# Kernel optimization log

Hardware: AMD Instinct MI355X
Metric: run time of the kernel (lower is better)

The kernel has to match this reference:

```python
import jax, jax.numpy as jnp
import numpy as np

D_MODEL = 1024
N_HEADS = 16
D_KV = 64
ROPE_THETA = 10000.0


def setup_inputs() -> dict:
    key = jax.random.key(0)
    k1, k2, k3, k4, k5 = jax.random.split(key, 5)
    B, S = 4, 2048
    scale = 0.02
    return {
        "positions": jnp.arange(S, dtype=jnp.int64 if jax.config.jax_enable_x64 else jnp.int32),
        "hidden_states": jax.random.normal(k1, (B, S, D_MODEL), dtype=jnp.float32),
        "wq": jax.random.normal(k2, (D_MODEL, N_HEADS * D_KV), dtype=jnp.float32) * scale,
        "wk": jax.random.normal(k3, (D_MODEL, N_HEADS * D_KV), dtype=jnp.float32) * scale,
        "wv": jax.random.normal(k4, (D_MODEL, N_HEADS * D_KV), dtype=jnp.float32) * scale,
        "wo": jax.random.normal(k5, (N_HEADS * D_KV, D_MODEL), dtype=jnp.float32) * scale,
    }


def _rope(positions, q, k):
    # Neox-style simple RoPE, matching SimpleRoPE fallback.
    # q, k: [B, H, S, Dh]
    Dh = q.shape[-1]
    inv_freq = 1.0 / (ROPE_THETA ** (jnp.arange(0, Dh, 2, dtype=jnp.float32) / Dh))  # [Dh/2]
    freqs = positions.astype(jnp.float32)[:, None] * inv_freq[None, :]  # [S, Dh/2]
    emb = jnp.concatenate([freqs, freqs], axis=-1)  # [S, Dh]
    cos = jnp.cos(emb)[None, None, :, :]
    sin = jnp.sin(emb)[None, None, :, :]

    def rotate_half(x):
        x1, x2 = jnp.split(x, 2, axis=-1)
        return jnp.concatenate([-x2, x1], axis=-1)

    q_rot = q * cos + rotate_half(q) * sin
    k_rot = k * cos + rotate_half(k) * sin
    return q_rot, k_rot


def reference(positions, hidden_states, wq, wk, wv, wo):
    B, S, _ = hidden_states.shape
    H, Dh = N_HEADS, D_KV

    def split_heads(x):  # [B, S, H*Dh] -> [B, H, S, Dh]
        return x.reshape(B, S, H, Dh).transpose(0, 2, 1, 3)

    q = split_heads(hidden_states @ wq)
    k = split_heads(hidden_states @ wk)
    v = split_heads(hidden_states @ wv)

    q, k = _rope(positions, q, k)

    # scale = 1.0 (no 1/sqrt(d) scaling), matching the source module
    scores = jnp.einsum("bhqd,bhkd->bhqk", q, k)
    attn = jax.nn.softmax(scores.astype(jnp.float32), axis=-1).astype(scores.dtype)
    # dropout is identity in eval mode
    out = jnp.einsum("bhqk,bhkd->bhqd", attn, v)  # [B, H, S, Dh]
    out = out.transpose(0, 2, 1, 3).reshape(B, S, H * Dh)
    return out @ wo
```

## Files before the change

### kernel.cpp

```cpp
#include <hip/hip_runtime.h>
#include <hip/hip_bf16.h>


typedef __bf16 bf16_t;
typedef __bf16 bf16x4 __attribute__((ext_vector_type(4)));
typedef __bf16 bf16x8 __attribute__((ext_vector_type(8)));
typedef float f32x4 __attribute__((ext_vector_type(4)));

#define MFMA16(a, b, c) __builtin_amdgcn_mfma_f32_16x16x32_bf16((a), (b), (c), 0, 0, 0)

#define GLOAD_LDS(gp, lp) \
  __builtin_amdgcn_global_load_lds( \
      (const __attribute__((address_space(1))) void*)(gp), \
      (__attribute__((address_space(3))) void*)(lp), 16, 0, 0)

__global__ __launch_bounds__(256) void cvt_kernel(const float* __restrict__ X,
                                                  bf16_t* __restrict__ Y) {
  const int i = (blockIdx.x * 256 + threadIdx.x) * 4;
  const f32x4 x = *(const f32x4*)(X + i);
  bf16x4 y;
#pragma unroll
  for (int k = 0; k < 4; k++) y[k] = (bf16_t)x[k];
  *(bf16x4*)(Y + i) = y;
}

__global__ __launch_bounds__(256) void wtrans4_kernel(
    const float* __restrict__ w0, const float* __restrict__ w1,
    const float* __restrict__ w2, const float* __restrict__ w3,
    bf16_t* __restrict__ out) {
  __shared__ bf16_t t[32][33];
  const int tx = threadIdx.x, ty = threadIdx.y;
  const int bx = blockIdx.x, by = blockIdx.y, z = blockIdx.z;
  const float* W = (z == 0) ? w0 : (z == 1) ? w1 : (z == 2) ? w2 : w3;
  bf16_t* Wt = out + (size_t)z * 1024 * 1024;
#pragma unroll
  for (int i = ty; i < 32; i += 8)
    t[i][tx] = (bf16_t)W[(size_t)(by * 32 + i) * 1024 + bx * 32 + tx];
  __syncthreads();
#pragma unroll
  for (int i = ty; i < 32; i += 8)
    Wt[(size_t)(bx * 32 + i) * 1024 + by * 32 + tx] = t[tx][i];
}

__global__ __launch_bounds__(256) void vtrans_kernel(const bf16_t* __restrict__ V,
                                                     bf16_t* __restrict__ VT) {
  __shared__ bf16_t t[32][33];
  const int tx = threadIdx.x, ty = threadIdx.y;
  const int sx = blockIdx.x * 32, cy = blockIdx.y * 32, b = blockIdx.z;
  const bf16_t* Vb = V + (size_t)b * 2048 * 1024;
  bf16_t* VTb = VT + (size_t)b * 1024 * 2048;
#pragma unroll
  for (int i = ty; i < 32; i += 8)
    t[i][tx] = Vb[(size_t)(sx + i) * 1024 + cy + tx];
  __syncthreads();
#pragma unroll
  for (int i = ty; i < 32; i += 8)
    VTb[(size_t)(cy + i) * 2048 + sx + tx] = t[tx][i];
}

template <typename TC, bool FUSED_QKV>
__global__ __launch_bounds__(256) void gemm_kernel(
    const bf16_t* __restrict__ A, const bf16_t* __restrict__ BtBase,
    TC* __restrict__ CBase, const int ropeIn) {
  constexpr int K = 1024, N = 1024;
  __shared__ __align__(16) bf16_t As[128 * 32];
  __shared__ __align__(16) bf16_t Bs[128 * 32];

  const int tid = threadIdx.x;
  const int lane = tid & 63, w = tid >> 6;
  const int l15 = lane & 15, quad = lane >> 4;
  const int wm = w >> 1, wn = w & 1;
  const int m0 = blockIdx.x * 128;

  int n0, rope;
  const bf16_t* Bt;
  TC* C;
  if (FUSED_QKV) {
    const int which = blockIdx.y >> 3;
    n0 = (blockIdx.y & 7) * 128;
    Bt = BtBase + (size_t)which * (1u << 20);
    C = CBase + (size_t)which * (8u << 20);
    rope = (which < 2);
  } else {
    n0 = blockIdx.y * 128;
    Bt = BtBase;
    C = CBase;
    rope = ropeIn;
  }

  f32x4 acc[4][4] = {};
  const int li8 = lane >> 3, j = lane & 7;

  for (int k0 = 0; k0 < K; k0 += 32) {
#pragma unroll
    for (int p = 0; p < 2; ++p) {
      const int g = w * 16 + p * 8 + li8;
      const int jp = j ^ (g & 7);
      const int row = 2 * g + (jp >> 2), kb = jp & 3;
      GLOAD_LDS(A + (size_t)(m0 + row) * K + k0 + kb * 8, As + (w * 16 + p * 8) * 64);
      GLOAD_LDS(Bt + (size_t)(n0 + row) * K + k0 + kb * 8, Bs + (w * 16 + p * 8) * 64);
    }
    __syncthreads();

    bf16x8 af[4], bfv[4];
#pragma unroll
    for (int mi = 0; mi < 4; mi++) {
      const int R = wm * 64 + mi * 16 + l15, g = R >> 1;
      const int jj = (((R & 1) << 2) | quad) ^ (g & 7);
      af[mi] = *(const bf16x8*)(As + g * 64 + jj * 8);
    }
#pragma unroll
    for (int ni = 0; ni < 4; ni++) {
      const int R = wn * 64 + ni * 16 + l15, g = R >> 1;
      const int jj = (((R & 1) << 2) | quad) ^ (g & 7);
      bfv[ni] = *(const bf16x8*)(Bs + g * 64 + jj * 8);
    }
#pragma unroll
    for (int mi = 0; mi < 4; mi++)
#pragma unroll
      for (int ni = 0; ni < 4; ni++)
        acc[mi][ni] = MFMA16(af[mi], bfv[ni], acc[mi][ni]);
    __syncthreads();
  }

#pragma unroll
  for (int mi = 0; mi < 4; mi++) {
    const int rbase = m0 + wm * 64 + mi * 16 + quad * 4;
    if (rope) {
#pragma unroll
      for (int r = 0; r < 4; r++) {
        const float pos = (float)((rbase + r) & 2047);
#pragma unroll
        for (int ni = 0; ni < 2; ni++) {
          const int d2 = ni * 16 + l15;
          const float invf = __powf(10000.0f, -(float)d2 * (1.0f / 32.0f));
          float sv, cv;
          __sincosf(pos * invf, &sv, &cv);
          const float a0 = acc[mi][ni][r], a2 = acc[mi][ni + 2][r];
          acc[mi][ni][r] = a0 * cv - a2 * sv;
          acc[mi][ni + 2][r] = a2 * cv + a0 * sv;
        }
      }
    }
#pragma unroll
    for (int ni = 0; ni < 4; ni++) {
      const int c0 = n0 + wn * 64 + ni * 16 + l15;
#pragma unroll
      for (int r = 0; r < 4; r++)
        C[(size_t)(rbase + r) * N + c0] = (TC)acc[mi][ni][r];
    }
  }
}

#define PSTR 72

__global__ __launch_bounds__(256) void attn_kernel(const bf16_t* __restrict__ Q,
                                                   const bf16_t* __restrict__ K,
                                                   const bf16_t* __restrict__ VT,
                                                   bf16_t* __restrict__ O) {
  __shared__ __align__(16) bf16_t Kl[64 * 64];
  __shared__ __align__(16) bf16_t Vl[64 * 64];
  __shared__ __align__(16) bf16_t Pl[4 * 16 * PSTR];

  const int tid = threadIdx.x;
  const int lane = tid & 63, w = tid >> 6;
  const int l15 = lane & 15, quad = lane >> 4;
  const int q0 = blockIdx.x * 64;
  const int bh = blockIdx.y, b = bh >> 4, h = bh & 15;

  const size_t base = (size_t)b * 2048 * 1024 + (size_t)h * 64;
  const bf16_t* Qb = Q + base;
  const bf16_t* Kb = K + base;
  const bf16_t* VTb = VT + (size_t)(b * 1024 + h * 64) * 2048;

  const int qrow = q0 + w * 16 + l15;
  bf16x8 qf[2];
  qf[0] = *(const bf16x8*)(Qb + (size_t)qrow * 1024 + quad * 8);
  qf[1] = *(const bf16x8*)(Qb + (size_t)qrow * 1024 + 32 + quad * 8);

  f32x4 accO[4] = {};
  float lsum[4] = {0.f, 0.f, 0.f, 0.f};

  const int li8 = lane >> 3, j = lane & 7;

  for (int kv0 = 0; kv0 < 2048; kv0 += 64) {
#pragma unroll
    for (int p = 0; p < 2; ++p) {
      const int kr = w * 16 + p * 8 + li8;
      const int blk = j ^ (kr & 7);
      GLOAD_LDS(Kb + (size_t)(kv0 + kr) * 1024 + blk * 8, Kl + (w * 16 + p * 8) * 64);
      GLOAD_LDS(VTb + (size_t)kr * 2048 + kv0 + blk * 8, Vl + (w * 16 + p * 8) * 64);
    }
    __syncthreads();

    f32x4 sc[4] = {};
#pragma unroll
    for (int t = 0; t < 2; t++)
#pragma unroll
      for (int nb = 0; nb < 4; nb++) {
        const int R = nb * 16 + l15;
        const int jj = (t * 4 + quad) ^ (R & 7);
        const bf16x8 kf = *(const bf16x8*)(Kl + R * 64 + jj * 8);
        sc[nb] = MFMA16(qf[t], kf, sc[nb]);
      }

#pragma unroll
    for (int nb = 0; nb < 4; nb++)
#pragma unroll
      for (int r = 0; r < 4; r++) {
        const float p = __expf(sc[nb][r]);
        lsum[r] += p;
        Pl[w * 16 * PSTR + (quad * 4 + r) * PSTR + nb * 16 + l15] = (bf16_t)p;
      }
    __asm__ volatile("s_waitcnt lgkmcnt(0)" ::: "memory");

#pragma unroll
    for (int t = 0; t < 2; t++) {
      const bf16x8 pf = *(const bf16x8*)(Pl + w * 16 * PSTR + l15 * PSTR + t * 32 + quad * 8);
#pragma unroll
      for (int nb = 0; nb < 4; nb++) {
        const int R = nb * 16 + l15;
        const int jj = (t * 4 + quad) ^ (R & 7);
        const bf16x8 vf = *(const bf16x8*)(Vl + R * 64 + jj * 8);
        accO[nb] = MFMA16(pf, vf, accO[nb]);
      }
    }
    __syncthreads();
  }

#pragma unroll
  for (int r = 0; r < 4; r++) {
    float s = lsum[r];
    s += __shfl_xor(s, 1);
    s += __shfl_xor(s, 2);
    s += __shfl_xor(s, 4);
    s += __shfl_xor(s, 8);
    lsum[r] = 1.0f / s;
  }
  bf16_t* Ob = O + base;
#pragma unroll
  for (int r = 0; r < 4; r++) {
    const int qr = q0 + w * 16 + quad * 4 + r;
#pragma unroll
    for (int nb = 0; nb < 4; nb++)
      Ob[(size_t)qr * 1024 + nb * 16 + l15] = (bf16_t)(accO[nb][r] * lsum[r]);
  }
}

extern "C" void kernel_launch(void* const* d_in, const int* in_sizes, int n_in,
                              void* d_out, int out_size, void* d_ws, size_t ws_size,
                              hipStream_t stream) {
  const float* hs = (const float*)d_in[1];
  const float* wq = (const float*)d_in[2];
  const float* wk = (const float*)d_in[3];
  const float* wv = (const float*)d_in[4];
  const float* wo = (const float*)d_in[5];

  char* ws = (char*)d_ws;
  const size_t MB = 1024 * 1024;
  bf16_t* WtQKV = (bf16_t*)(ws + 0 * MB);
  bf16_t* WtO = (bf16_t*)(ws + 6 * MB);
  bf16_t* hsb = (bf16_t*)(ws + 8 * MB);
  bf16_t* VT = (bf16_t*)(ws + 8 * MB);
  bf16_t* Qw = (bf16_t*)(ws + 24 * MB);
  bf16_t* Kw = (bf16_t*)(ws + 40 * MB);
  bf16_t* Vw = (bf16_t*)(ws + 56 * MB);
  bf16_t* Ow = (bf16_t*)(ws + 56 * MB);

  wtrans4_kernel<<<dim3(32, 32, 4), dim3(32, 8), 0, stream>>>(wq, wk, wv, wo, WtQKV);
  cvt_kernel<<<8192, 256, 0, stream>>>(hs, hsb);

  gemm_kernel<bf16_t, true><<<dim3(64, 24), 256, 0, stream>>>(hsb, WtQKV, Qw, 0);

  vtrans_kernel<<<dim3(64, 32, 4), dim3(32, 8), 0, stream>>>(Vw, VT);

  attn_kernel<<<dim3(32, 64), 256, 0, stream>>>(Qw, Kw, VT, Ow);

  gemm_kernel<float, false><<<dim3(64, 8), 256, 0, stream>>>(Ow, WtO, (float*)d_out, 0);
}
```

Measured before the change: 339.9 us.

## Split attention KV across waves with 128-wide tiles and LDS cross-wave reduction

The attention kernel now processes 128 KV rows per iteration, and each of the four waves handles a 32-row KV slice for all 64 queries of the block instead of owning 16 queries. K fragments are reused across four query sub-blocks. Partial outputs and row sums are combined through a shared LDS arena with a rotating accumulation followed by normalisation. This halves the number of loop iterations and barriers and improves MFMA-to-load reuse, but it adds register pressure (a 4x4 accumulator array, with launch_bounds set to 2 blocks), a cross-wave reduction epilogue, and a larger LDS footprint.

New measurement: 931.0 us. +173.9%, slower.

```diff
diff --git a/kernel.cpp b/kernel.cpp
--- a/kernel.cpp
+++ b/kernel.cpp
@@ -152,19 +152,23 @@
   }
 }
 
-#define PSTR 72
-
-__global__ __launch_bounds__(256) void attn_kernel(const bf16_t* __restrict__ Q,
-                                                   const bf16_t* __restrict__ K,
-                                                   const bf16_t* __restrict__ VT,
-                                                   bf16_t* __restrict__ O) {
-  __shared__ __align__(16) bf16_t Kl[64 * 64];
-  __shared__ __align__(16) bf16_t Vl[64 * 64];
-  __shared__ __align__(16) bf16_t Pl[4 * 16 * PSTR];
+#define PLSTR 40
+
+__global__ __launch_bounds__(256, 2) void attn_kernel(const bf16_t* __restrict__ Q,
+                                                      const bf16_t* __restrict__ K,
+                                                      const bf16_t* __restrict__ VT,
+                                                      bf16_t* __restrict__ O) {
+  __shared__ __align__(16) char arena[53248];
+  bf16_t* Kl = (bf16_t*)arena;
+  bf16_t* Vl = (bf16_t*)(arena + 16384);
+  bf16_t* Pl = (bf16_t*)(arena + 32768);
+  float* Obuf = (float*)arena;
+  float* lsumB = (float*)(arena + 32768);
 
   const int tid = threadIdx.x;
   const int lane = tid & 63, w = tid >> 6;
   const int l15 = lane & 15, quad = lane >> 4;
+  const int li8 = lane >> 3, j = lane & 7;
   const int q0 = blockIdx.x * 64;
   const int bh = blockIdx.y, b = bh >> 4, h = bh & 15;
 
@@ -173,77 +177,119 @@
   const bf16_t* Kb = K + base;
   const bf16_t* VTb = VT + (size_t)(b * 1024 + h * 64) * 2048;
 
-  const int qrow = q0 + w * 16 + l15;
-  bf16x8 qf[2];
-  qf[0] = *(const bf16x8*)(Qb + (size_t)qrow * 1024 + quad * 8);
-  qf[1] = *(const bf16x8*)(Qb + (size_t)qrow * 1024 + 32 + quad * 8);
-
-  f32x4 accO[4] = {};
-  float lsum[4] = {0.f, 0.f, 0.f, 0.f};
-
-  const int li8 = lane >> 3, j = lane & 7;
-
-  for (int kv0 = 0; kv0 < 2048; kv0 += 64) {
-#pragma unroll
-    for (int p = 0; p < 2; ++p) {
-      const int kr = w * 16 + p * 8 + li8;
-      const int blk = j ^ (kr & 7);
-      GLOAD_LDS(Kb + (size_t)(kv0 + kr) * 1024 + blk * 8, Kl + (w * 16 + p * 8) * 64);
-      GLOAD_LDS(VTb + (size_t)kr * 2048 + kv0 + blk * 8, Vl + (w * 16 + p * 8) * 64);
-    }
-    __syncthreads();
-
-    f32x4 sc[4] = {};
+  bf16x8 qf[4][2];
+#pragma unroll
+  for (int mb = 0; mb < 4; mb++)
 #pragma unroll
     for (int t = 0; t < 2; t++)
-#pragma unroll
-      for (int nb = 0; nb < 4; nb++) {
-        const int R = nb * 16 + l15;
+      qf[mb][t] = *(const bf16x8*)(Qb + (size_t)(q0 + mb * 16 + l15) * 1024 + t * 32 + quad * 8);
+
+  f32x4 accO[4][4] = {};
+  float lsum[4][4] = {};
+  bf16_t* Plw = Pl + w * (64 * PLSTR);
+
+  for (int kv0 = 0; kv0 < 2048; kv0 += 128) {
+#pragma unroll
+    for (int p = 0; p < 4; ++p) {
+      const int g = w * 32 + p * 8 + li8;
+      const int blk = j ^ (g & 7);
+      GLOAD_LDS(Kb + (size_t)(kv0 + g) * 1024 + blk * 8, Kl + (w * 32 + p * 8) * 64);
+      GLOAD_LDS(VTb + (size_t)(g >> 1) * 2048 + kv0 + (g & 1) * 64 + blk * 8,
+                Vl + (w * 32 + p * 8) * 64);
+    }
+    __syncthreads();
+
+#pragma unroll
+    for (int nb2 = 0; nb2 < 2; nb2++) {
+      f32x4 sc[4] = {};
+#pragma unroll
+      for (int t = 0; t < 2; t++) {
+        const int R = w * 32 + nb2 * 16 + l15;
         const int jj = (t * 4 + quad) ^ (R & 7);
         const bf16x8 kf = *(const bf16x8*)(Kl + R * 64 + jj * 8);
-        sc[nb] = MFMA16(qf[t], kf, sc[nb]);
+#pragma unroll
+        for (int mb = 0; mb < 4; mb++)
+          sc[mb] = MFMA16(qf[mb][t], kf, sc[mb]);
       }
-
-#pragma unroll
-    for (int nb = 0; nb < 4; nb++)
-#pragma unroll
-      for (int r = 0; r < 4; r++) {
-        const float p = __expf(sc[nb][r]);
-        lsum[r] += p;
-        Pl[w * 16 * PSTR + (quad * 4 + r) * PSTR + nb * 16 + l15] = (bf16_t)p;
-      }
+#pragma unroll
+      for (int mb = 0; mb < 4; mb++)
+#pragma unroll
+        for (int r = 0; r < 4; r++) {
+          const float p = __expf(sc[mb][r]);
+          lsum[mb][r] += p;
+          Plw[(mb * 16 + quad * 4 + r) * PLSTR + nb2 * 16 + l15] = (bf16_t)p;
+        }
+    }
     __asm__ volatile("s_waitcnt lgkmcnt(0)" ::: "memory");
 
-#pragma unroll
-    for (int t = 0; t < 2; t++) {
-      const bf16x8 pf = *(const bf16x8*)(Pl + w * 16 * PSTR + l15 * PSTR + t * 32 + quad * 8);
-#pragma unroll
-      for (int nb = 0; nb < 4; nb++) {
-        const int R = nb * 16 + l15;
-        const int jj = (t * 4 + quad) ^ (R & 7);
-        const bf16x8 vf = *(const bf16x8*)(Vl + R * 64 + jj * 8);
-        accO[nb] = MFMA16(pf, vf, accO[nb]);
-      }
-    }
-    __syncthreads();
-  }
-
-#pragma unroll
-  for (int r = 0; r < 4; r++) {
-    float s = lsum[r];
-    s += __shfl_xor(s, 1);
-    s += __shfl_xor(s, 2);
-    s += __shfl_xor(s, 4);
-    s += __shfl_xor(s, 8);
-    lsum[r] = 1.0f / s;
-  }
+    bf16x8 pf[4], vf[4];
+#pragma unroll
+    for (int mb = 0; mb < 4; mb++)
+      pf[mb] = *(const bf16x8*)(Plw + (mb * 16 + l15) * PLSTR + quad * 8);
+#pragma unroll
+    for (int nb = 0; nb < 4; nb++) {
+      const int R = nb * 16 + l15;
+      const int g = R * 2 + (w >> 1);
+      const int jj = ((w & 1) * 4 + quad) ^ (g & 7);
+      vf[nb] = *(const bf16x8*)(Vl + g * 64 + jj * 8);
+    }
+#pragma unroll
+    for (int mb = 0; mb < 4; mb++)
+#pragma unroll
+      for (int nb = 0; nb < 4; nb++)
+        accO[mb][nb] = MFMA16(pf[mb], vf[nb], accO[mb][nb]);
+    __syncthreads();
+  }
+
+#pragma unroll
+  for (int mb = 0; mb < 4; mb++)
+#pragma unroll
+    for (int r = 0; r < 4; r++) {
+      float s = lsum[mb][r];
+      s += __shfl_xor(s, 1);
+      s += __shfl_xor(s, 2);
+      s += __shfl_xor(s, 4);
+      s += __shfl_xor(s, 8);
+      lsum[mb][r] = s;
+    }
+  if (l15 == 0) {
+#pragma unroll
+    for (int mb = 0; mb < 4; mb++)
+#pragma unroll
+      for (int r = 0; r < 4; r++)
+        lsumB[w * 64 + mb * 16 + quad * 4 + r] = lsum[mb][r];
+  }
+
+#pragma unroll
+  for (int p = 0; p < 4; p++) {
+    const int s = (w + p) & 3;
+    if (p == 0) {
+#pragma unroll
+      for (int nb = 0; nb < 4; nb++)
+#pragma unroll
+        for (int r = 0; r < 4; r++)
+          Obuf[(s * 16 + quad * 4 + r) * 68 + nb * 16 + l15] = accO[s][nb][r];
+    } else {
+#pragma unroll
+      for (int nb = 0; nb < 4; nb++)
+#pragma unroll
+        for (int r = 0; r < 4; r++)
+          Obuf[(s * 16 + quad * 4 + r) * 68 + nb * 16 + l15] += accO[s][nb][r];
+    }
+    __syncthreads();
+  }
+
   bf16_t* Ob = O + base;
 #pragma unroll
-  for (int r = 0; r < 4; r++) {
-    const int qr = q0 + w * 16 + quad * 4 + r;
-#pragma unroll
-    for (int nb = 0; nb < 4; nb++)
-      Ob[(size_t)qr * 1024 + nb * 16 + l15] = (bf16_t)(accO[nb][r] * lsum[r]);
+  for (int rr = 0; rr < 4; rr++) {
+    const int row = w * 16 + rr * 4 + quad;
+    const f32x4 o = *(const f32x4*)(Obuf + row * 68 + l15 * 4);
+    const float inv =
+        1.0f / (lsumB[row] + lsumB[64 + row] + lsumB[128 + row] + lsumB[192 + row]);
+    bf16x4 ob;
+#pragma unroll
+    for (int c = 0; c < 4; c++) ob[c] = (bf16_t)(o[c] * inv);
+    *(bf16x4*)(Ob + (size_t)(q0 + row) * 1024 + l15 * 4) = ob;
   }
 }
 
```
